# Optimization experiments

Hardware: AMD Instinct MI355X
Metric: run time of the kernel (lower is better)

The kernel has to match this reference:

```python
import jax, jax.numpy as jnp
import numpy as np

DN3D = ('NCDHW', 'OIDHW', 'NCDHW')

def conv_t3d(x, w, stride):
    # PyTorch ConvTranspose3d with padding=0: w is (C_in, C_out, k1,k2,k3).
    # Equivalent dilated conv: flip spatial dims, swap in/out channels,
    # lhs_dilation=stride, padding k-1 on each side.
    wf = jnp.flip(w, axis=(2, 3, 4)).transpose(1, 0, 2, 3, 4)  # (O, I, k, k, k)
    pad = [(k - 1, k - 1) for k in w.shape[2:]]
    dn = jax.lax.conv_dimension_numbers(x.shape, wf.shape, DN3D)
    return jax.lax.conv_general_dilated(x, wf, (1, 1, 1), pad,
                                        lhs_dilation=stride, dimension_numbers=dn)

def conv3d(x, w, stride, pad):
    dn = jax.lax.conv_dimension_numbers(x.shape, w.shape, DN3D)
    return jax.lax.conv_general_dilated(x, w, stride, [(pad, pad)] * 3,
                                        dimension_numbers=dn)

def setup_inputs() -> dict:
    key = jax.random.key(0)
    ks = jax.random.split(key, 7)
    out_ch, emb, p = 4, 256, 8
    B, T, D = 2, 8, 4  # batch, 4th spatial dim, coarse grid (input_size//patch_size)
    s = 0.05
    return {
        'x':  jax.random.normal(ks[0], (B, T, out_ch * emb, D, D, D), jnp.float32),
        'w1': jax.random.normal(ks[1], (out_ch * emb, out_ch * 2, p // 2, p // 2, p // 2), jnp.float32) * s,
        'b1': jax.random.normal(ks[2], (out_ch * 2,), jnp.float32) * s,
        'w2': jax.random.normal(ks[3], (out_ch * 2, out_ch * 2, 4, 4, 4), jnp.float32) * s,
        'b2': jax.random.normal(ks[4], (out_ch * 2,), jnp.float32) * s,
        'w3': jax.random.normal(ks[5], (out_ch, out_ch * 2, 4, 4, 4), jnp.float32) * s,
        'b3': jax.random.normal(ks[6], (out_ch,), jnp.float32) * s,
    }

def reference(x, w1, b1, w2, b2, w3, b3):
    # x: (B, D4, C_in, D1, D2, D3). All 4D kernels are size/stride 1 along D4,
    # so fold D4 into the batch and run 3D (de)convs.
    B, T, C, D, _, _ = x.shape
    h = x.reshape(B * T, C, D, D, D)
    bcast = lambda b: b[None, :, None, None, None]
    h = jnp.tanh(conv_t3d(h, w1, (4, 4, 4)) + bcast(b1))   # -> (BT, 8, 16,16,16)
    h = jnp.tanh(conv_t3d(h, w2, (4, 4, 4)) + bcast(b2))   # -> (BT, 8, 64,64,64)
    h = conv3d(h, w3, (2, 2, 2), 1) + bcast(b3)             # -> (BT, 4, 32,32,32)
    out = h.reshape(B, T, *h.shape[1:])                     # (B, D4, C, 32,32,32)
    return jnp.moveaxis(out, 1, -1)                         # (B, C, 32,32,32, D4)
```

## Files before the change

kernel.cpp:

```cpp
#include <hip/hip_runtime.h>
#include <cstdint>

typedef _Float16 f16x8 __attribute__((ext_vector_type(8)));
typedef float f32x4 __attribute__((ext_vector_type(4)));
typedef _Float16 half2_t __attribute__((ext_vector_type(2)));

__device__ __forceinline__ unsigned pkh2(float a, float b) {
  return __builtin_bit_cast(unsigned, __builtin_amdgcn_cvt_pkrtz(a, b));
}
__device__ __forceinline__ float fast_tanh(float x) {
  float e = __builtin_amdgcn_exp2f(x * 2.885390081777927f);
  return 1.0f - 2.0f * __builtin_amdgcn_rcpf(e + 1.0f);
}

#if __has_builtin(__builtin_amdgcn_fdot2)
__device__ __forceinline__ float dot2h(unsigned a, unsigned b, float c) {
  return __builtin_amdgcn_fdot2(__builtin_bit_cast(half2_t, a),
                                __builtin_bit_cast(half2_t, b), c, false);
}
#else
__device__ __forceinline__ float dot2h(unsigned a, unsigned b, float c) {
  half2_t av = __builtin_bit_cast(half2_t, a);
  half2_t bv = __builtin_bit_cast(half2_t, b);
  c = fmaf((float)av.x, (float)bv.x, c);
  c = fmaf((float)av.y, (float)bv.y, c);
  return c;
}
#endif

template <int ITERS>
__global__ __launch_bounds__(256, 4) void k_stage1(const float* __restrict__ x,
                                                   const float* __restrict__ w1,
                                                   const float* __restrict__ w3,
                                                   float* __restrict__ part,
                                                   unsigned* __restrict__ wtab) {
  constexpr int NS = 32 / ITERS;
  constexpr int KSB = (NS == 8) ? 3 : (NS == 4) ? 2 : (NS == 2) ? 1 : 0;
  __shared__ __align__(16) char lds_raw[64 * 65 * 4];
  unsigned short* As = (unsigned short*)lds_raw;
  unsigned short* Bs = (unsigned short*)(lds_raw + 5120);
  float* Cs = (float*)lds_raw;

  const int tid = threadIdx.x;
  if (blockIdx.x == 0) {
    int l = tid << 2;
#pragma unroll
    for (int j = 0; j < 4; ++j) {
      int d = l + j;
      int slot = d & 3, chU = (d >> 2) & 1, kh = (d >> 3) & 3,
          kd = (d >> 5) & 3, cio = d >> 7;
      int co = (chU << 1) + (slot & 1);
      int kwb = (slot >> 1) << 1;
      int base = ((co << 3) + cio) * 64 + (kd << 4) + (kh << 2) + kwb;
      wtab[d] = pkh2(w3[base], w3[base + 1]);
    }
  }

  const int ks = blockIdx.x & (NS - 1);
  const int bt = (blockIdx.x >> KSB) & 15;
  const int co = blockIdx.x >> (KSB + 4);
  const int w = tid >> 6, lane = tid & 63, lm = lane & 15, q = lane >> 4;
  const int rrow = tid & 63, kgr = tid >> 6;

  f32x4 acc[4];
#pragma unroll
  for (int i = 0; i < 4; ++i) acc[i] = (f32x4){0.f, 0.f, 0.f, 0.f};

  const float* gA = x + (bt << 16) + ((size_t)(ks * ITERS * 32) << 6);
  const float* gB = w1 + (co << 6) + (size_t)(ks * ITERS * 32) * 512;

  float va[2][8], vb[2][8];
#define S1_LOAD(buf, it)                            \
  {                                                 \
    const int kb = (it) * 32 + (kgr << 3);          \
    _Pragma("unroll") for (int j = 0; j < 8; ++j) { \
      va[buf][j] = gA[((kb + j) << 6) | rrow];      \
      vb[buf][j] = gB[(kb + j) * 512 + rrow];       \
    }                                               \
  }
  S1_LOAD(0, 0);
#pragma unroll
  for (int it = 0; it < ITERS; ++it) {
    const int cur = it & 1;
    if (it + 1 < ITERS) S1_LOAD(cur ^ 1, it + 1);
    uint4 pa, pb;
    pa.x = pkh2(va[cur][0], va[cur][1]);
    pa.y = pkh2(va[cur][2], va[cur][3]);
    pa.z = pkh2(va[cur][4], va[cur][5]);
    pa.w = pkh2(va[cur][6], va[cur][7]);
    pb.x = pkh2(vb[cur][0], vb[cur][1]);
    pb.y = pkh2(vb[cur][2], vb[cur][3]);
    pb.z = pkh2(vb[cur][4], vb[cur][5]);
    pb.w = pkh2(vb[cur][6], vb[cur][7]);
    *(uint4*)&As[rrow * 40 + (kgr << 3)] = pa;
    *(uint4*)&Bs[rrow * 40 + (kgr << 3)] = pb;
    __syncthreads();
    f16x8 a = *(const f16x8*)&As[((w << 4) + lm) * 40 + (q << 3)];
#pragma unroll
    for (int nf = 0; nf < 4; ++nf) {
      f16x8 b = *(const f16x8*)&Bs[((nf << 4) + lm) * 40 + (q << 3)];
      acc[nf] = __builtin_amdgcn_mfma_f32_16x16x32_f16(a, b, acc[nf], 0, 0, 0);
    }
    __syncthreads();
  }
#undef S1_LOAD
#pragma unroll
  for (int nf = 0; nf < 4; ++nf)
#pragma unroll
    for (int r = 0; r < 4; ++r) {
      int m = (w << 4) + (q << 2) + r;
      int n = (nf << 4) + lm;
      Cs[m * 65 + n] = acc[nf][r];
    }
  __syncthreads();
  float* dst = part + (((size_t)(((ks << 4) + bt) << 3) + co) << 12);
#pragma unroll
  for (int j = 0; j < 4; ++j) {
    int pos = (tid << 2) + (j << 10);
    int z = pos >> 8, y = (pos >> 4) & 15, xx = pos & 15;
    int m = ((z >> 2) << 4) + ((y >> 2) << 2) + (xx >> 2);
    int n = ((z & 3) << 4) + ((y & 3) << 2);
    float4 v;
    v.x = Cs[m * 65 + n + 0];
    v.y = Cs[m * 65 + n + 1];
    v.z = Cs[m * 65 + n + 2];
    v.w = Cs[m * 65 + n + 3];
    *(float4*)&dst[pos] = v;
  }
}

template <int NSPLIT>
__global__ __launch_bounds__(512) void k_stage23(
    const float* __restrict__ part, const float* __restrict__ w2,
    const float* __restrict__ b2, const float* __restrict__ b3,
    const float* __restrict__ b1, const unsigned* __restrict__ wtab,
    float* __restrict__ out) {
  __shared__ __align__(16) unsigned win_d[2][18 * 34 * 12];
  __shared__ __align__(16) unsigned h1p[6 * 240];
  __shared__ __align__(16) unsigned w2p[8 * 320];

  const int tid = threadIdx.x;
  const int bid = blockIdx.x;
  const int bt = bid & 15;
  const int tile = bid >> 4;
  const int tz = tile >> 3, ty = (tile >> 2) & 1, tx = tile & 3;
  const int Z0 = tz << 3, Y0 = ty << 4, X0 = tx << 3;
  const int Qz0 = (Z0 << 1) - 1, Qy0 = (Y0 << 1) - 1, Qx0 = (X0 << 1) - 1;
  const int Uz0 = (tz << 2) - 1, Uy0 = (ty << 3) - 1, Ux0 = (tx << 2) - 1;

  float sv[6][NSPLIT];
  float b1v[6];
  int dsto[6];
  bool inb[6];
#pragma unroll
  for (int k = 0; k < 6; ++k) {
    int l = tid + (k << 9);
    bool vld = l < 2880;
    int ll = vld ? l : 0;
    int ci = ll / 360;
    int sp = ll - ci * 360;
    int ux = sp % 6;
    int t1 = sp / 6;
    int uy = t1 % 10;
    int uz = t1 / 10;
    int gz = Uz0 + uz, gy = Uy0 + uy, gx = Ux0 + ux;
    inb[k] = vld && (unsigned)gz < 16u && (unsigned)gy < 16u &&
             (unsigned)gx < 16u;
    dsto[k] = vld ? (uz * 480 + uy * 48 + (ux << 3) + ci) : -1;
    b1v[k] = 0.f;
    if (inb[k]) {
      b1v[k] = b1[ci];
      const float* p =
          part + (((size_t)(bt << 3) + ci) << 12) + (gz << 8) + (gy << 4) + gx;
#pragma unroll
      for (int sg = 0; sg < NSPLIT; ++sg) sv[k][sg] = p[(size_t)sg << 19];
    }
  }

  for (int l = tid; l < 2048; l += 512) {
    int j = l & 3, kx = (l >> 2) & 3, kzy = (l >> 4) & 15, cio = l >> 8;
    int kpos = (kzy << 2) + kx;
    float w0 = w2[(((j << 1) << 3) + cio) * 64 + kpos];
    float w1v = w2[((((j << 1) + 1) << 3) + cio) * 64 + kpos];
    w2p[cio * 320 + kzy * 20 + (kx << 2) + j] = pkh2(w0, w1v);
  }
  for (int u = tid; u < 1224; u += 512) {
    int wz = u / 68;
    int rem = u - wz * 68;
    int wy = rem >> 1;
    int half = rem & 1;
    int qz = Qz0 + wz, qy = Qy0 + wy;
    if ((unsigned)qz < 64u && (unsigned)qy < 64u) continue;
    uint4 zz;
    zz.x = zz.y = zz.z = zz.w = 0u;
#pragma unroll
    for (int bsel = 0; bsel < 2; ++bsel) {
      unsigned* wrow = win_d[bsel] + (wz * 34 + wy) * 12;
      if (half == 0) {
        *(uint4*)wrow = zz;
      } else {
        *(uint4*)(wrow + 4) = zz;
        wrow[8] = 0u;
      }
    }
  }

#pragma unroll
  for (int k = 0; k < 6; ++k) {
    if (dsto[k] < 0) continue;
    float v = 0.f;
    if (inb[k]) {
      float s = b1v[k];
#pragma unroll
      for (int sg = 0; sg < NSPLIT; ++sg) s += sv[k][sg];
      v = fast_tanh(s);
    }
    ((_Float16*)h1p)[dsto[k]] = (_Float16)v;
  }

  int fu_row[3], fu_h1[3], fu_w2[3], fu_half[3];
  bool fu_act[3];
#pragma unroll
  for (int k = 0; k < 3; ++k) {
    int u = tid + (k << 9);
    bool act = u < 1224;
    int uu = act ? u : 0;
    int wz = uu / 68;
    int rem = uu - wz * 68;
    int wy = rem >> 1, half = rem & 1;
    int qz = Qz0 + wz, qy = Qy0 + wy;
    fu_act[k] = act && (unsigned)qz < 64u && (unsigned)qy < 64u;
    fu_row[k] = (wz * 34 + wy) * 12;
    int kz = qz & 3, ky = qy & 3;
    fu_w2[k] = ((kz << 2) + ky) * 20;
    int uzp = (qz >> 2) - Uz0, uyp = (qy >> 2) - Uy0;
    fu_h1[k] = uzp * 240 + uyp * 24;
    fu_half[k] = half;
  }
  const bool gLo = (Qx0 >= 0), gHi = (Qx0 + 17 < 64);

  __syncthreads();

  float acc[2][4];
#pragma unroll
  for (int a = 0; a < 2; ++a)
#pragma unroll
    for (int i = 0; i < 4; ++i) acc[a][i] = 0.f;

  const int xh = tid & 1, yq = (tid >> 1) & 15, zq = (tid >> 5) & 7;
  const int chS = __builtin_amdgcn_readfirstlane(tid >> 8);

  for (int cio = 0; cio < 8; ++cio) {
    unsigned* wbuf = win_d[cio & 1];
    const float b2c = b2[cio];
#pragma unroll
    for (int k = 0; k < 3; ++k) {
      if (!fu_act[k]) continue;
      unsigned* wrow = wbuf + fu_row[k];
      const unsigned* w2b = w2p + cio * 320 + fu_w2[k];
      uint4 wv[4];
#pragma unroll
      for (int kx = 0; kx < 4; ++kx) wv[kx] = *(const uint4*)(w2b + (kx << 2));
      const unsigned* h1b = h1p + fu_h1[k];
#define DOT8(hc, kx)                                            \
  dot2h((hc).w, wv[kx].w,                                       \
        dot2h((hc).z, wv[kx].z,                                 \
              dot2h((hc).y, wv[kx].y, dot2h((hc).x, wv[kx].x, b2c))))
      if (fu_half[k] == 0) {
        uint4 h0 = *(const uint4*)(h1b);
        uint4 h1c = *(const uint4*)(h1b + 4);
        uint4 h2c = *(const uint4*)(h1b + 8);
        float vals[8];
        vals[0] = gLo ? fast_tanh(DOT8(h0, 3)) : 0.f;
#pragma unroll
        for (int kx = 0; kx < 4; ++kx) vals[1 + kx] = fast_tanh(DOT8(h1c, kx));
#pragma unroll
        for (int kx = 0; kx < 3; ++kx) vals[5 + kx] = fast_tanh(DOT8(h2c, kx));
        uint4 s0;
        s0.x = pkh2(vals[0], vals[1]);
        s0.y = pkh2(vals[2], vals[3]);
        s0.z = pkh2(vals[4], vals[5]);
        s0.w = pkh2(vals[6], vals[7]);
        *(uint4*)wrow = s0;
      } else {
        uint4 h2c = *(const uint4*)(h1b + 8);
        uint4 h3 = *(const uint4*)(h1b + 12);
        uint4 h4 = *(const uint4*)(h1b + 16);
        uint4 h5 = *(const uint4*)(h1b + 20);
        float vals[10];
        vals[0] = fast_tanh(DOT8(h2c, 3));
#pragma unroll
        for (int kx = 0; kx < 4; ++kx) vals[1 + kx] = fast_tanh(DOT8(h3, kx));
#pragma unroll
        for (int kx = 0; kx < 4; ++kx) vals[5 + kx] = fast_tanh(DOT8(h4, kx));
        vals[9] = gHi ? fast_tanh(DOT8(h5, 0)) : 0.f;
        uint4 s1;
        s1.x = pkh2(vals[0], vals[1]);
        s1.y = pkh2(vals[2], vals[3]);
        s1.z = pkh2(vals[4], vals[5]);
        s1.w = pkh2(vals[6], vals[7]);
        *(uint4*)(wrow + 4) = s1;
        wrow[8] = pkh2(vals[8], vals[9]);
      }
#undef DOT8
    }
    __syncthreads();
#pragma unroll
    for (int kd = 0; kd < 4; ++kd) {
      int wz = (zq << 1) + kd;
#pragma unroll
      for (int kh = 0; kh < 4; ++kh) {
        int wy = (yq << 1) + kh;
        const unsigned* rowp = wbuf + (wz * 34 + wy) * 12 + (xh << 2);
        uint4 rv = *(const uint4*)rowp;
        unsigned r4 = rowp[4];
        unsigned r[5] = {rv.x, rv.y, rv.z, rv.w, r4};
        const uint4 wv =
            *(const uint4*)&wtab[((((cio << 4) + (kd << 2) + kh) << 1) + chS)
                                 << 2];
        unsigned wA[2] = {wv.x, wv.y};
        unsigned wB[2] = {wv.z, wv.w};
#pragma unroll
        for (int cc = 0; cc < 2; ++cc) {
#pragma unroll
          for (int i = 0; i < 4; ++i) {
            float a0 = dot2h(r[i], wA[cc], acc[cc][i]);
            acc[cc][i] = dot2h(r[i + 1], wB[cc], a0);
          }
        }
      }
    }
  }
  const int ch = tid >> 8;
  const int b = bt >> 3, t8 = bt & 7;
  const int z = Z0 + zq;
  const int y = Y0 + yq;
#pragma unroll
  for (int cc = 0; cc < 2; ++cc) {
    int c4 = (ch << 1) + cc;
    float bias = b3[c4];
#pragma unroll
    for (int i = 0; i < 4; ++i) {
      int xx = X0 + (xh << 2) + i;
      out[(((((b << 2) + c4) * 32 + z) * 32 + y) * 32 + xx) << 3 | t8] =
          acc[cc][i] + bias;
    }
  }
}

extern "C" void kernel_launch(void* const* d_in, const int* in_sizes, int n_in,
                              void* d_out, int out_size, void* d_ws,
                              size_t ws_size, hipStream_t stream) {
  (void)in_sizes; (void)n_in; (void)out_size;
  const float* x = (const float*)d_in[0];
  const float* w1 = (const float*)d_in[1];
  const float* b1 = (const float*)d_in[2];
  const float* w2 = (const float*)d_in[3];
  const float* b2 = (const float*)d_in[4];
  const float* w3 = (const float*)d_in[5];
  const float* b3 = (const float*)d_in[6];
  float* out = (float*)d_out;
  float* part = (float*)d_ws;

  const size_t plane = (size_t)16 * 8 * 4096;
  int nsplit = 1;
  if (ws_size >= 4 * plane * 4 + 4096)
    nsplit = 4;
  else if (ws_size >= 2 * plane * 4 + 4096)
    nsplit = 2;
  unsigned* wtab = (unsigned*)(part + (size_t)nsplit * plane);

  switch (nsplit) {
    case 4:
      k_stage1<8><<<dim3(512), dim3(256), 0, stream>>>(x, w1, w3, part, wtab);
      k_stage23<4><<<dim3(512), dim3(512), 0, stream>>>(part, w2, b2, b3, b1,
                                                        wtab, out);
      break;
    case 2:
      k_stage1<16><<<dim3(256), dim3(256), 0, stream>>>(x, w1, w3, part, wtab);
      k_stage23<2><<<dim3(512), dim3(512), 0, stream>>>(part, w2, b2, b3, b1,
                                                        wtab, out);
      break;
    default:
      k_stage1<32><<<dim3(128), dim3(256), 0, stream>>>(x, w1, w3, part, wtab);
      k_stage23<1><<<dim3(512), dim3(512), 0, stream>>>(part, w2, b2, b3, b1,
                                                        wtab, out);
      break;
  }
}
```

Measured before the change: 140.7 us.

## Halve stage-2/3 tile depth, single-buffer window, one output channel per thread

The fused stage-2/3 kernel now works on tiles half as deep in z, so it launches twice as many blocks. Each thread computes one output channel instead of two. The double-buffered window is replaced by a single buffer with a barrier at the end of each input channel, and launch bounds ask for higher occupancy. This cuts shared memory and registers per block to fit more blocks per CU, at the cost of more halo recompute of the stage-2 tanh values, an extra barrier per channel, and a per-thread weight select. The dot2 fallback also becomes inline asm, but it only applies when the builtin is unavailable.

```diff
diff --git a/kernel.cpp b/kernel.cpp
--- a/kernel.cpp
+++ b/kernel.cpp
@@ -20,11 +20,9 @@
 }
 #else
 __device__ __forceinline__ float dot2h(unsigned a, unsigned b, float c) {
-  half2_t av = __builtin_bit_cast(half2_t, a);
-  half2_t bv = __builtin_bit_cast(half2_t, b);
-  c = fmaf((float)av.x, (float)bv.x, c);
-  c = fmaf((float)av.y, (float)bv.y, c);
-  return c;
+  float d;
+  asm("v_dot2_f32_f16 %0, %1, %2, %3" : "=v"(d) : "v"(a), "v"(b), "v"(c));
+  return d;
 }
 #endif
 
@@ -130,35 +128,37 @@
 }
 
 template <int NSPLIT>
-__global__ __launch_bounds__(512) void k_stage23(
+__global__ __launch_bounds__(512, 8) void k_stage23(
     const float* __restrict__ part, const float* __restrict__ w2,
     const float* __restrict__ b2, const float* __restrict__ b3,
     const float* __restrict__ b1, const unsigned* __restrict__ wtab,
     float* __restrict__ out) {
-  __shared__ __align__(16) unsigned win_d[2][18 * 34 * 12];
-  __shared__ __align__(16) unsigned h1p[6 * 240];
+  __shared__ __align__(16) unsigned win[10 * 34 * 12];
+  __shared__ __align__(16) unsigned h1p[960];
   __shared__ __align__(16) unsigned w2p[8 * 320];
 
   const int tid = threadIdx.x;
   const int bid = blockIdx.x;
-  const int bt = bid & 15;
-  const int tile = bid >> 4;
-  const int tz = tile >> 3, ty = (tile >> 2) & 1, tx = tile & 3;
-  const int Z0 = tz << 3, Y0 = ty << 4, X0 = tx << 3;
+  const int tile = bid & 63;
+  const int bt = bid >> 6;
+  const int tz = tile & 7;
+  const int tyx = tile >> 3;
+  const int ty = tyx >> 2, tx = tyx & 3;
+  const int Z0 = tz << 2, Y0 = ty << 4, X0 = tx << 3;
   const int Qz0 = (Z0 << 1) - 1, Qy0 = (Y0 << 1) - 1, Qx0 = (X0 << 1) - 1;
-  const int Uz0 = (tz << 2) - 1, Uy0 = (ty << 3) - 1, Ux0 = (tx << 2) - 1;
-
-  float sv[6][NSPLIT];
-  float b1v[6];
-  int dsto[6];
-  bool inb[6];
-#pragma unroll
-  for (int k = 0; k < 6; ++k) {
+  const int Uz0 = Qz0 >> 2, Uy0 = Qy0 >> 2, Ux0 = Qx0 >> 2;
+
+  float sv[4][NSPLIT];
+  float b1v[4];
+  int dsto[4];
+  bool inb[4];
+#pragma unroll
+  for (int k = 0; k < 4; ++k) {
     int l = tid + (k << 9);
-    bool vld = l < 2880;
+    bool vld = l < 1920;
     int ll = vld ? l : 0;
-    int ci = ll / 360;
-    int sp = ll - ci * 360;
+    int ci = ll / 240;
+    int sp = ll - ci * 240;
     int ux = sp % 6;
     int t1 = sp / 6;
     int uy = t1 % 10;
@@ -184,7 +184,7 @@
     float w1v = w2[((((j << 1) + 1) << 3) + cio) * 64 + kpos];
     w2p[cio * 320 + kzy * 20 + (kx << 2) + j] = pkh2(w0, w1v);
   }
-  for (int u = tid; u < 1224; u += 512) {
+  for (int u = tid; u < 680; u += 512) {
     int wz = u / 68;
     int rem = u - wz * 68;
     int wy = rem >> 1;
@@ -193,20 +193,17 @@
     if ((unsigned)qz < 64u && (unsigned)qy < 64u) continue;
     uint4 zz;
     zz.x = zz.y = zz.z = zz.w = 0u;
-#pragma unroll
-    for (int bsel = 0; bsel < 2; ++bsel) {
-      unsigned* wrow = win_d[bsel] + (wz * 34 + wy) * 12;
-      if (half == 0) {
-        *(uint4*)wrow = zz;
-      } else {
-        *(uint4*)(wrow + 4) = zz;
-        wrow[8] = 0u;
-      }
-    }
-  }
-
-#pragma unroll
-  for (int k = 0; k < 6; ++k) {
+    unsigned* wrow = win + (wz * 34 + wy) * 12;
+    if (half == 0) {
+      *(uint4*)wrow = zz;
+    } else {
+      *(uint4*)(wrow + 4) = zz;
+      wrow[8] = 0u;
+    }
+  }
+
+#pragma unroll
+  for (int k = 0; k < 4; ++k) {
     if (dsto[k] < 0) continue;
     float v = 0.f;
     if (inb[k]) {
@@ -218,12 +215,12 @@
     ((_Float16*)h1p)[dsto[k]] = (_Float16)v;
   }
 
-  int fu_row[3], fu_h1[3], fu_w2[3], fu_half[3];
-  bool fu_act[3];
-#pragma unroll
-  for (int k = 0; k < 3; ++k) {
+  int fu_row[2], fu_h1[2], fu_w2[2], fu_half[2];
+  bool fu_act[2];
+#pragma unroll
+  for (int k = 0; k < 2; ++k) {
     int u = tid + (k << 9);
-    bool act = u < 1224;
+    bool act = u < 680;
     int uu = act ? u : 0;
     int wz = uu / 68;
     int rem = uu - wz * 68;
@@ -241,22 +238,20 @@
 
   __syncthreads();
 
-  float acc[2][4];
-#pragma unroll
-  for (int a = 0; a < 2; ++a)
-#pragma unroll
-    for (int i = 0; i < 4; ++i) acc[a][i] = 0.f;
-
-  const int xh = tid & 1, yq = (tid >> 1) & 15, zq = (tid >> 5) & 7;
-  const int chS = __builtin_amdgcn_readfirstlane(tid >> 8);
+  float acc[4];
+#pragma unroll
+  for (int i = 0; i < 4; ++i) acc[i] = 0.f;
+
+  const int xh = tid & 1, yq = (tid >> 1) & 15, zq = (tid >> 5) & 3;
+  const int chS = __builtin_amdgcn_readfirstlane(tid >> 7);
+  const int chU = chS >> 1, sel = chS & 1;
 
   for (int cio = 0; cio < 8; ++cio) {
-    unsigned* wbuf = win_d[cio & 1];
     const float b2c = b2[cio];
 #pragma unroll
-    for (int k = 0; k < 3; ++k) {
+    for (int k = 0; k < 2; ++k) {
       if (!fu_act[k]) continue;
-      unsigned* wrow = wbuf + fu_row[k];
+      unsigned* wrow = win + fu_row[k];
       const unsigned* w2b = w2p + cio * 320 + fu_w2[k];
       uint4 wv[4];
 #pragma unroll
@@ -311,40 +306,33 @@
 #pragma unroll
       for (int kh = 0; kh < 4; ++kh) {
         int wy = (yq << 1) + kh;
-        const unsigned* rowp = wbuf + (wz * 34 + wy) * 12 + (xh << 2);
+        const unsigned* rowp = win + (wz * 34 + wy) * 12 + (xh << 2);
         uint4 rv = *(const uint4*)rowp;
         unsigned r4 = rowp[4];
         unsigned r[5] = {rv.x, rv.y, rv.z, rv.w, r4};
         const uint4 wv =
-            *(const uint4*)&wtab[((((cio << 4) + (kd << 2) + kh) << 1) + chS)
+            *(const uint4*)&wtab[((((cio << 4) + (kd << 2) + kh) << 1) | chU)
                                  << 2];
-        unsigned wA[2] = {wv.x, wv.y};
-        unsigned wB[2] = {wv.z, wv.w};
-#pragma unroll
-        for (int cc = 0; cc < 2; ++cc) {
-#pragma unroll
-          for (int i = 0; i < 4; ++i) {
-            float a0 = dot2h(r[i], wA[cc], acc[cc][i]);
-            acc[cc][i] = dot2h(r[i + 1], wB[cc], a0);
-          }
+        unsigned wA = sel ? wv.y : wv.x;
+        unsigned wB = sel ? wv.w : wv.z;
+#pragma unroll
+        for (int i = 0; i < 4; ++i) {
+          float a0 = dot2h(r[i], wA, acc[i]);
+          acc[i] = dot2h(r[i + 1], wB, a0);
         }
       }
     }
-  }
-  const int ch = tid >> 8;
+    __syncthreads();
+  }
   const int b = bt >> 3, t8 = bt & 7;
   const int z = Z0 + zq;
   const int y = Y0 + yq;
-#pragma unroll
-  for (int cc = 0; cc < 2; ++cc) {
-    int c4 = (ch << 1) + cc;
-    float bias = b3[c4];
-#pragma unroll
-    for (int i = 0; i < 4; ++i) {
-      int xx = X0 + (xh << 2) + i;
-      out[(((((b << 2) + c4) * 32 + z) * 32 + y) * 32 + xx) << 3 | t8] =
-          acc[cc][i] + bias;
-    }
+  const float bias = b3[chS];
+#pragma unroll
+  for (int i = 0; i < 4; ++i) {
+    int xx = X0 + (xh << 2) + i;
+    out[(((((b << 2) + chS) * 32 + z) * 32 + y) * 32 + xx) << 3 | t8] =
+        acc[i] + bias;
   }
 }
 
@@ -373,18 +361,18 @@
   switch (nsplit) {
     case 4:
       k_stage1<8><<<dim3(512), dim3(256), 0, stream>>>(x, w1, w3, part, wtab);
-      k_stage23<4><<<dim3(512), dim3(512), 0, stream>>>(part, w2, b2, b3, b1,
-                                                        wtab, out);
+      k_stage23<4><<<dim3(1024), dim3(512), 0, stream>>>(part, w2, b2, b3, b1,
+                                                         wtab, out);
       break;
     case 2:
       k_stage1<16><<<dim3(256), dim3(256), 0, stream>>>(x, w1, w3, part, wtab);
-      k_stage23<2><<<dim3(512), dim3(512), 0, stream>>>(part, w2, b2, b3, b1,
-                                                        wtab, out);
+      k_stage23<2><<<dim3(1024), dim3(512), 0, stream>>>(part, w2, b2, b3, b1,
+                                                         wtab, out);
       break;
     default:
       k_stage1<32><<<dim3(128), dim3(256), 0, stream>>>(x, w1, w3, part, wtab);
-      k_stage23<1><<<dim3(512), dim3(512), 0, stream>>>(part, w2, b2, b3, b1,
-                                                        wtab, out);
+      k_stage23<1><<<dim3(1024), dim3(512), 0, stream>>>(part, w2, b2, b3, b1,
+                                                         wtab, out);
       break;
   }
 }
```

New measurement: 144.4 us. 2.6% more time.

## Use single padded LDS window and reuse rows across two output z-planes

Applied to the files above, without the earlier changes.

Replaces the double-buffered stride-12 window with a single stride-13 padded window, which cuts shared memory and avoids LDS bank conflicts, at the cost of an extra barrier per channel iteration and scalar (non-vector) LDS accesses. The stage-3 thread mapping changes so each thread computes one output channel for two adjacent z planes, reusing each loaded window row for both planes. Block index ordering is swapped (tile-major within bt), launch bounds gain an occupancy hint, and the fallback dot2 uses inline asm.

```diff
diff --git a/kernel.cpp b/kernel.cpp
--- a/kernel.cpp
+++ b/kernel.cpp
@@ -20,11 +20,9 @@
 }
 #else
 __device__ __forceinline__ float dot2h(unsigned a, unsigned b, float c) {
-  half2_t av = __builtin_bit_cast(half2_t, a);
-  half2_t bv = __builtin_bit_cast(half2_t, b);
-  c = fmaf((float)av.x, (float)bv.x, c);
-  c = fmaf((float)av.y, (float)bv.y, c);
-  return c;
+  float d;
+  asm("v_dot2_f32_f16 %0, %1, %2, %3" : "=v"(d) : "v"(a), "v"(b), "v"(c));
+  return d;
 }
 #endif
 
@@ -130,23 +128,24 @@
 }
 
 template <int NSPLIT>
-__global__ __launch_bounds__(512) void k_stage23(
+__global__ __launch_bounds__(512, 4) void k_stage23(
     const float* __restrict__ part, const float* __restrict__ w2,
     const float* __restrict__ b2, const float* __restrict__ b3,
     const float* __restrict__ b1, const unsigned* __restrict__ wtab,
     float* __restrict__ out) {
-  __shared__ __align__(16) unsigned win_d[2][18 * 34 * 12];
+  __shared__ unsigned win13[18 * 34 * 13];
   __shared__ __align__(16) unsigned h1p[6 * 240];
   __shared__ __align__(16) unsigned w2p[8 * 320];
 
   const int tid = threadIdx.x;
   const int bid = blockIdx.x;
-  const int bt = bid & 15;
-  const int tile = bid >> 4;
-  const int tz = tile >> 3, ty = (tile >> 2) & 1, tx = tile & 3;
+  const int tile = bid & 31;
+  const int bt = bid >> 5;
+  const int tz = tile >> 3;
+  const int ty = (tile >> 2) & 1, tx = tile & 3;
   const int Z0 = tz << 3, Y0 = ty << 4, X0 = tx << 3;
   const int Qz0 = (Z0 << 1) - 1, Qy0 = (Y0 << 1) - 1, Qx0 = (X0 << 1) - 1;
-  const int Uz0 = (tz << 2) - 1, Uy0 = (ty << 3) - 1, Ux0 = (tx << 2) - 1;
+  const int Uz0 = Qz0 >> 2, Uy0 = Qy0 >> 2, Ux0 = Qx0 >> 2;
 
   float sv[6][NSPLIT];
   float b1v[6];
@@ -191,17 +190,11 @@
     int half = rem & 1;
     int qz = Qz0 + wz, qy = Qy0 + wy;
     if ((unsigned)qz < 64u && (unsigned)qy < 64u) continue;
-    uint4 zz;
-    zz.x = zz.y = zz.z = zz.w = 0u;
-#pragma unroll
-    for (int bsel = 0; bsel < 2; ++bsel) {
-      unsigned* wrow = win_d[bsel] + (wz * 34 + wy) * 12;
-      if (half == 0) {
-        *(uint4*)wrow = zz;
-      } else {
-        *(uint4*)(wrow + 4) = zz;
-        wrow[8] = 0u;
-      }
+    unsigned* wrow = win13 + (wz * 34 + wy) * 13;
+    if (half == 0) {
+      wrow[0] = 0u; wrow[1] = 0u; wrow[2] = 0u; wrow[3] = 0u;
+    } else {
+      wrow[4] = 0u; wrow[5] = 0u; wrow[6] = 0u; wrow[7] = 0u; wrow[8] = 0u;
     }
   }
 
@@ -230,7 +223,7 @@
     int wy = rem >> 1, half = rem & 1;
     int qz = Qz0 + wz, qy = Qy0 + wy;
     fu_act[k] = act && (unsigned)qz < 64u && (unsigned)qy < 64u;
-    fu_row[k] = (wz * 34 + wy) * 12;
+    fu_row[k] = (wz * 34 + wy) * 13;
     int kz = qz & 3, ky = qy & 3;
     fu_w2[k] = ((kz << 2) + ky) * 20;
     int uzp = (qz >> 2) - Uz0, uyp = (qy >> 2) - Uy0;
@@ -247,16 +240,16 @@
 #pragma unroll
     for (int i = 0; i < 4; ++i) acc[a][i] = 0.f;
 
-  const int xh = tid & 1, yq = (tid >> 1) & 15, zq = (tid >> 5) & 7;
-  const int chS = __builtin_amdgcn_readfirstlane(tid >> 8);
+  const int xh = tid & 1, yq = (tid >> 1) & 15, zp = (tid >> 5) & 3;
+  const int chS = __builtin_amdgcn_readfirstlane(tid >> 7);
+  const int chU = chS >> 1, sel = chS & 1;
 
   for (int cio = 0; cio < 8; ++cio) {
-    unsigned* wbuf = win_d[cio & 1];
     const float b2c = b2[cio];
 #pragma unroll
     for (int k = 0; k < 3; ++k) {
       if (!fu_act[k]) continue;
-      unsigned* wrow = wbuf + fu_row[k];
+      unsigned* wrow = win13 + fu_row[k];
       const unsigned* w2b = w2p + cio * 320 + fu_w2[k];
       uint4 wv[4];
 #pragma unroll
@@ -276,12 +269,10 @@
         for (int kx = 0; kx < 4; ++kx) vals[1 + kx] = fast_tanh(DOT8(h1c, kx));
 #pragma unroll
         for (int kx = 0; kx < 3; ++kx) vals[5 + kx] = fast_tanh(DOT8(h2c, kx));
-        uint4 s0;
-        s0.x = pkh2(vals[0], vals[1]);
-        s0.y = pkh2(vals[2], vals[3]);
-        s0.z = pkh2(vals[4], vals[5]);
-        s0.w = pkh2(vals[6], vals[7]);
-        *(uint4*)wrow = s0;
+        wrow[0] = pkh2(vals[0], vals[1]);
+        wrow[1] = pkh2(vals[2], vals[3]);
+        wrow[2] = pkh2(vals[4], vals[5]);
+        wrow[3] = pkh2(vals[6], vals[7]);
       } else {
         uint4 h2c = *(const uint4*)(h1b + 8);
         uint4 h3 = *(const uint4*)(h1b + 12);
@@ -294,56 +285,64 @@
 #pragma unroll
         for (int kx = 0; kx < 4; ++kx) vals[5 + kx] = fast_tanh(DOT8(h4, kx));
         vals[9] = gHi ? fast_tanh(DOT8(h5, 0)) : 0.f;
-        uint4 s1;
-        s1.x = pkh2(vals[0], vals[1]);
-        s1.y = pkh2(vals[2], vals[3]);
-        s1.z = pkh2(vals[4], vals[5]);
-        s1.w = pkh2(vals[6], vals[7]);
-        *(uint4*)(wrow + 4) = s1;
+        wrow[4] = pkh2(vals[0], vals[1]);
+        wrow[5] = pkh2(vals[2], vals[3]);
+        wrow[6] = pkh2(vals[4], vals[5]);
+        wrow[7] = pkh2(vals[6], vals[7]);
         wrow[8] = pkh2(vals[8], vals[9]);
       }
 #undef DOT8
     }
     __syncthreads();
 #pragma unroll
-    for (int kd = 0; kd < 4; ++kd) {
-      int wz = (zq << 1) + kd;
-#pragma unroll
-      for (int kh = 0; kh < 4; ++kh) {
-        int wy = (yq << 1) + kh;
-        const unsigned* rowp = wbuf + (wz * 34 + wy) * 12 + (xh << 2);
-        uint4 rv = *(const uint4*)rowp;
-        unsigned r4 = rowp[4];
-        unsigned r[5] = {rv.x, rv.y, rv.z, rv.w, r4};
-        const uint4 wv =
-            *(const uint4*)&wtab[((((cio << 4) + (kd << 2) + kh) << 1) + chS)
-                                 << 2];
-        unsigned wA[2] = {wv.x, wv.y};
-        unsigned wB[2] = {wv.z, wv.w};
-#pragma unroll
-        for (int cc = 0; cc < 2; ++cc) {
+    for (int kh = 0; kh < 4; ++kh) {
+      const int wy = (yq << 1) + kh;
+      uint4 wvk[4];
+#pragma unroll
+      for (int kd = 0; kd < 4; ++kd)
+        wvk[kd] = *(const uint4*)&wtab[((((cio << 4) + (kd << 2) + kh) << 1) |
+                                        chU)
+                                       << 2];
+      int rowdw = ((zp << 2) * 34 + wy) * 13 + (xh << 2);
+#pragma unroll
+      for (int wzi = 0; wzi < 6; ++wzi) {
+        unsigned r[5];
+#pragma unroll
+        for (int j = 0; j < 5; ++j) r[j] = win13[rowdw + j];
+        if (wzi <= 3) {
+          unsigned wA = sel ? wvk[wzi].y : wvk[wzi].x;
+          unsigned wB = sel ? wvk[wzi].w : wvk[wzi].z;
 #pragma unroll
           for (int i = 0; i < 4; ++i) {
-            float a0 = dot2h(r[i], wA[cc], acc[cc][i]);
-            acc[cc][i] = dot2h(r[i + 1], wB[cc], a0);
+            float a0 = dot2h(r[i], wA, acc[0][i]);
+            acc[0][i] = dot2h(r[i + 1], wB, a0);
           }
         }
+        if (wzi >= 2) {
+          unsigned wA = sel ? wvk[wzi - 2].y : wvk[wzi - 2].x;
+          unsigned wB = sel ? wvk[wzi - 2].w : wvk[wzi - 2].z;
+#pragma unroll
+          for (int i = 0; i < 4; ++i) {
+            float a0 = dot2h(r[i], wA, acc[1][i]);
+            acc[1][i] = dot2h(r[i + 1], wB, a0);
+          }
+        }
+        rowdw += 34 * 13;
       }
     }
-  }
-  const int ch = tid >> 8;
+    if (cio < 7) __syncthreads();
+  }
   const int b = bt >> 3, t8 = bt & 7;
-  const int z = Z0 + zq;
   const int y = Y0 + yq;
-#pragma unroll
-  for (int cc = 0; cc < 2; ++cc) {
-    int c4 = (ch << 1) + cc;
-    float bias = b3[c4];
+  const float bias = b3[chS];
+#pragma unroll
+  for (int dz = 0; dz < 2; ++dz) {
+    int z = Z0 + (zp << 1) + dz;
 #pragma unroll
     for (int i = 0; i < 4; ++i) {
       int xx = X0 + (xh << 2) + i;
-      out[(((((b << 2) + c4) * 32 + z) * 32 + y) * 32 + xx) << 3 | t8] =
-          acc[cc][i] + bias;
+      out[(((((b << 2) + chS) * 32 + z) * 32 + y) * 32 + xx) << 3 | t8] =
+          acc[dz][i] + bias;
     }
   }
 }
```

Measured after the change: 310.1 us. 2.2x slower.
